# Kernel tuning notes

Measured on AMD Instinct MI355X. Metric: run time of the kernel, lower is better.

Reference implementation:

```python
import jax, jax.numpy as jnp
import numpy as np

VEC, HID, B, S = 1280, 128, 4, 256
EPS = 1e-5


def _ln(x):
    m = x.mean(-1, keepdims=True)
    v = ((x - m) ** 2).mean(-1, keepdims=True)
    return (x - m) / jnp.sqrt(v + EPS)


def _add_attn(q_in, kv_in, Wq, Wk, wv):
    # Additive (Bahdanau) attention: scores[b,i,j] = wv . tanh(q[b,i] + k[b,j])
    q = q_in @ Wq            # [B, Sq, H]
    k = kv_in @ Wk           # [B, Sk, H]
    feat = jnp.tanh(q[:, :, None, :] + k[:, None, :, :])   # [B, Sq, Sk, H]
    scores = jnp.einsum('bijh,h->bij', feat, wv)
    attn = jax.nn.softmax(scores, axis=-1)
    return jnp.einsum('bij,bjd->bid', attn, kv_in)          # values = kv_in


def _res_fc(x, W1, b1, W2, b2):
    return jnp.maximum(x @ W1 + b1, 0.0) @ W2 + b2 + x


def setup_inputs() -> dict:
    key = jax.random.key(0)
    ks = iter(jax.random.split(key, 64))
    d = {
        'X': jax.random.normal(next(ks), (B, S, VEC), dtype=jnp.float32),
        'lys_pos': 100,
    }
    sc = 0.02
    for i in (1, 2, 3, 4):
        d[f'Wq{i}'] = jax.random.normal(next(ks), (VEC, HID), dtype=jnp.float32) * sc
        d[f'Wk{i}'] = jax.random.normal(next(ks), (VEC, HID), dtype=jnp.float32) * sc
        d[f'wv{i}'] = jax.random.normal(next(ks), (HID,), dtype=jnp.float32) * sc
    for i in (1, 2, 3):
        d[f'rW1_{i}'] = jax.random.normal(next(ks), (VEC, HID), dtype=jnp.float32) * sc
        d[f'rb1_{i}'] = jnp.zeros((HID,), dtype=jnp.float32)
        d[f'rW2_{i}'] = jax.random.normal(next(ks), (HID, VEC), dtype=jnp.float32) * sc
        d[f'rb2_{i}'] = jnp.zeros((VEC,), dtype=jnp.float32)
    d['hW1'] = jax.random.normal(next(ks), (VEC, 32), dtype=jnp.float32) * sc
    d['hb1'] = jnp.zeros((32,), dtype=jnp.float32)
    d['hW2'] = jax.random.normal(next(ks), (32, 12), dtype=jnp.float32) * sc
    d['hb2'] = jnp.zeros((12,), dtype=jnp.float32)
    d['hW3'] = jax.random.normal(next(ks), (12, 2), dtype=jnp.float32) * sc
    d['hb3'] = jnp.zeros((2,), dtype=jnp.float32)
    return d


def reference(X, lys_pos,
              Wq1, Wk1, wv1, Wq2, Wk2, wv2, Wq3, Wk3, wv3, Wq4, Wk4, wv4,
              rW1_1, rb1_1, rW2_1, rb2_1,
              rW1_2, rb1_2, rW2_2, rb2_2,
              rW1_3, rb1_3, rW2_3, rb2_3,
              hW1, hb1, hW2, hb2, hW3, hb3):
    X = X.astype(jnp.float32)
    X = _ln(_add_attn(X, X, Wq1, Wk1, wv1) + X)
    X = _res_fc(X, rW1_1, rb1_1, rW2_1, rb2_1)
    X = _ln(_add_attn(X, X, Wq2, Wk2, wv2) + X)
    X = _res_fc(X, rW1_2, rb1_2, rW2_2, rb2_2)
    X = _ln(_add_attn(X, X, Wq3, Wk3, wv3) + X)
    X = _res_fc(X, rW1_3, rb1_3, rW2_3, rb2_3)
    X_lys = X[:, lys_pos, :][:, None, :]                    # [B, 1, VEC]
    X_lys = _ln(_add_attn(X_lys, X, Wq4, Wk4, wv4) + X_lys)
    h = jnp.maximum(X_lys @ hW1 + hb1, 0.0)                 # dropout = identity (eval)
    h = jnp.maximum(h @ hW2 + hb2, 0.0)
    logits = (h @ hW3 + hb3)[:, 0, :]                       # squeeze(1) -> [B, 2]
    return logits
```

## Files before the change

kernel.cpp:

```cpp
#include <hip/hip_runtime.h>


#define DEV __device__ __forceinline__

static constexpr int VEC = 1280;
static constexpr int HID = 128;
static constexpr int BB  = 4;
static constexpr int SS  = 256;
static constexpr int MROWS = BB * SS;
static constexpr int NPART = 8;

DEV float ftanh(float x) {
  float e = __expf(2.0f * x);
  return 1.0f - __fdividef(2.0f, e + 1.0f);
}

DEV float waveSum(float v) {
#pragma unroll
  for (int off = 32; off > 0; off >>= 1) v += __shfl_xor(v, off, 64);
  return v;
}
DEV float waveMax(float v) {
#pragma unroll
  for (int off = 32; off > 0; off >>= 1) v = fmaxf(v, __shfl_xor(v, off, 64));
  return v;
}
DEV float blockSum(float v, float* red) {
  v = waveSum(v);
  int tid = threadIdx.x;
  if ((tid & 63) == 0) red[tid >> 6] = v;
  __syncthreads();
  float r = (red[0] + red[1]) + (red[2] + red[3]);
  __syncthreads();
  return r;
}
DEV float blockMax(float v, float* red) {
  v = waveMax(v);
  int tid = threadIdx.x;
  if ((tid & 63) == 0) red[tid >> 6] = v;
  __syncthreads();
  float r = fmaxf(fmaxf(red[0], red[1]), fmaxf(red[2], red[3]));
  __syncthreads();
  return r;
}

template <int MODE, bool AFUSE, bool OBIAS, bool ORES>
__global__ __launch_bounds__(256) void gemm_k(
    const float* __restrict__ A, long sAb, long aPart,
    const float* __restrict__ B0, const float* __restrict__ B1, int nSplitB,
    long sBb, int ldB,
    float* __restrict__ C, long sCb,
    const float* __restrict__ aBias, const float* __restrict__ oBias,
    const float* __restrict__ res,
    int N, int K, int kChunk) {
  const int n0 = blockIdx.x * 64;
  const int m0 = blockIdx.y * 64;
  const int z  = blockIdx.z;

  const float* Ab = A + (MODE == 2 ? (long)z * sAb : 0L);
  float*       Cb = C + (MODE >= 1 ? (long)z * sCb : 0L);
  const float* resz = ORES ? (res + (MODE == 2 ? (long)z * sCb : 0L)) : nullptr;
  const float* Bsel;
  int nb;
  if (n0 < nSplitB) { Bsel = B0; nb = n0; } else { Bsel = B1; nb = n0 - nSplitB; }
  if (MODE == 2) Bsel += (long)z * sBb;

  const int kBeg = (MODE == 1) ? z * kChunk : 0;
  const int kEnd = (MODE == 1) ? kBeg + kChunk : K;

  __shared__ float As[16][68];
  __shared__ float Bs[16][68];

  const int tid = threadIdx.x;
  const int tx = tid & 15, ty = tid >> 4;
  const int ar = tid >> 2, ac = (tid & 3) << 2;
  const int br = tid >> 4, bc = (tid & 15) << 2;

  auto loadA = [&](int kt) -> float4 {
    const size_t aoff = (size_t)(m0 + ar) * K + kt + ac;
    if (AFUSE) {
      float4 s = *(const float4*)(Ab + aoff);
#pragma unroll
      for (int p = 1; p < NPART; ++p) {
        const float4 t = *(const float4*)(Ab + (long)p * aPart + aoff);
        s.x += t.x; s.y += t.y; s.z += t.z; s.w += t.w;
      }
      const float4 bz = *(const float4*)(aBias + kt + ac);
      s.x = fmaxf(s.x + bz.x, 0.0f);
      s.y = fmaxf(s.y + bz.y, 0.0f);
      s.z = fmaxf(s.z + bz.z, 0.0f);
      s.w = fmaxf(s.w + bz.w, 0.0f);
      return s;
    }
    return *(const float4*)(Ab + aoff);
  };
  auto loadB = [&](int kt) -> float4 {
    return *(const float4*)(Bsel + (size_t)(kt + br) * ldB + nb + bc);
  };

  float acc[4][4] = {};
  float4 a4 = loadA(kBeg);
  float4 b4 = loadB(kBeg);

  for (int kt = kBeg; kt < kEnd; kt += 16) {
    __syncthreads();
    As[ac + 0][ar] = a4.x;
    As[ac + 1][ar] = a4.y;
    As[ac + 2][ar] = a4.z;
    As[ac + 3][ar] = a4.w;
    *(float4*)&Bs[br][bc] = b4;
    __syncthreads();
    if (kt + 16 < kEnd) {
      a4 = loadA(kt + 16);
      b4 = loadB(kt + 16);
    }
#pragma unroll
    for (int kk = 0; kk < 16; ++kk) {
      const float4 av = *(const float4*)&As[kk][ty << 2];
      const float4 bv = *(const float4*)&Bs[kk][tx << 2];
      const float a[4] = {av.x, av.y, av.z, av.w};
      const float b[4] = {bv.x, bv.y, bv.z, bv.w};
#pragma unroll
      for (int i = 0; i < 4; ++i)
#pragma unroll
        for (int j = 0; j < 4; ++j) acc[i][j] = fmaf(a[i], b[j], acc[i][j]);
    }
  }

#pragma unroll
  for (int i = 0; i < 4; ++i) {
    const int m = m0 + (ty << 2) + i;
#pragma unroll
    for (int j = 0; j < 4; ++j) {
      const int n = n0 + (tx << 2) + j;
      float v = acc[i][j];
      if (OBIAS) v += oBias[n];
      if (ORES) v += resz[(size_t)m * N + n];
      Cb[(size_t)m * N + n] = v;
    }
  }
}

__global__ __launch_bounds__(256) void qksum_k(const float* __restrict__ QKp,
                                               long ps,
                                               float* __restrict__ Qd,
                                               float* __restrict__ KT) {
  const int r = blockIdx.x, tid = threadIdx.x;
  const int b = r >> 8, j = r & 255;
  const size_t off = (size_t)r * 256 + tid;
  float v = 0.0f;
#pragma unroll
  for (int p = 0; p < NPART; ++p) v += QKp[(long)p * ps + off];
  if (tid < 128) {
    Qd[(size_t)r * 128 + tid] = v;
  } else {
    KT[(size_t)b * 32768 + (size_t)(tid - 128) * 256 + j] = v;
  }
}

__global__ __launch_bounds__(256) void scores2_k(const float* __restrict__ Qd,
                                                 const float* __restrict__ KT,
                                                 const float* __restrict__ wv,
                                                 float* __restrict__ attn) {
  const int b = blockIdx.y, i0 = blockIdx.x * 2, tid = threadIdx.x;
  __shared__ float qs[2][128], wvs[128], red[4];
  {
    const int rr = tid >> 7, h = tid & 127;
    qs[rr][h] = Qd[(size_t)(b * 256 + i0 + rr) * 128 + h];
  }
  if (tid < 128) wvs[tid] = wv[tid];
  __syncthreads();

  const float* KTb = KT + (size_t)b * 32768 + tid;
  float s0 = 0.0f, s1 = 0.0f;
#pragma unroll 4
  for (int h = 0; h < 128; h += 4) {
    const float k0 = KTb[(h + 0) * 256];
    const float k1 = KTb[(h + 1) * 256];
    const float k2 = KTb[(h + 2) * 256];
    const float k3 = KTb[(h + 3) * 256];
    const float w0 = wvs[h], w1 = wvs[h + 1], w2 = wvs[h + 2], w3 = wvs[h + 3];
    s0 += w0 * ftanh(qs[0][h] + k0) + w1 * ftanh(qs[0][h + 1] + k1) +
          w2 * ftanh(qs[0][h + 2] + k2) + w3 * ftanh(qs[0][h + 3] + k3);
    s1 += w0 * ftanh(qs[1][h] + k0) + w1 * ftanh(qs[1][h + 1] + k1) +
          w2 * ftanh(qs[1][h + 2] + k2) + w3 * ftanh(qs[1][h + 3] + k3);
  }
  {
    const float mx = blockMax(s0, red);
    const float e = __expf(s0 - mx);
    const float tot = blockSum(e, red);
    attn[(size_t)(b * 256 + i0) * 256 + tid] = e / tot;
  }
  {
    const float mx = blockMax(s1, red);
    const float e = __expf(s1 - mx);
    const float tot = blockSum(e, red);
    attn[(size_t)(b * 256 + i0 + 1) * 256 + tid] = e / tot;
  }
}

__global__ __launch_bounds__(256) void ln1_k(const float* __restrict__ A,
                                             float* __restrict__ Y) {
  __shared__ float red[4];
  const int r = blockIdx.x, tid = threadIdx.x;
  const float* a = A + (size_t)r * VEC;
  float v[5];
  float sum = 0.0f;
#pragma unroll
  for (int k = 0; k < 5; ++k) {
    v[k] = a[tid + k * 256];
    sum += v[k];
  }
  sum = blockSum(sum, red);
  const float m = sum * (1.0f / VEC);
  float sq = 0.0f;
#pragma unroll
  for (int k = 0; k < 5; ++k) {
    const float dl = v[k] - m;
    sq += dl * dl;
  }
  sq = blockSum(sq, red);
  const float rstd = rsqrtf(sq * (1.0f / VEC) + 1e-5f);
  float* y = Y + (size_t)r * VEC;
#pragma unroll
  for (int k = 0; k < 5; ++k) y[tid + k * 256] = (v[k] - m) * rstd;
}

__global__ __launch_bounds__(256) void scores4_k(const float* __restrict__ Qd,
                                                 const float* __restrict__ KT,
                                                 const float* __restrict__ wv4,
                                                 const int* __restrict__ lys,
                                                 float* __restrict__ aw4) {
  const int b = blockIdx.x, tid = threadIdx.x;
  __shared__ float qs[128], wvs[128], red[4];
  const int lp = lys[0];
  if (tid < 128) {
    qs[tid] = Qd[(size_t)(b * 256 + lp) * 128 + tid];
    wvs[tid] = wv4[tid];
  }
  __syncthreads();
  const float* KTb = KT + (size_t)b * 32768 + tid;
  float s = 0.0f;
#pragma unroll 4
  for (int h = 0; h < 128; h += 4) {
    s += wvs[h + 0] * ftanh(qs[h + 0] + KTb[(h + 0) * 256]);
    s += wvs[h + 1] * ftanh(qs[h + 1] + KTb[(h + 1) * 256]);
    s += wvs[h + 2] * ftanh(qs[h + 2] + KTb[(h + 2) * 256]);
    s += wvs[h + 3] * ftanh(qs[h + 3] + KTb[(h + 3) * 256]);
  }
  const float mx = blockMax(s, red);
  const float e = __expf(s - mx);
  const float tot = blockSum(e, red);
  aw4[b * 256 + tid] = e / tot;
}

__global__ __launch_bounds__(256) void pv4_k(const float* __restrict__ aw4,
                                             const float* __restrict__ X3,
                                             const int* __restrict__ lys,
                                             float* __restrict__ A4) {
  const int b = blockIdx.x, c = blockIdx.y * 256 + threadIdx.x;
  __shared__ float aws[256];
  aws[threadIdx.x] = aw4[b * 256 + threadIdx.x];
  __syncthreads();
  const float* Xb = X3 + (size_t)b * SS * VEC;
  float acc = 0.0f;
#pragma unroll 8
  for (int j = 0; j < 256; ++j) acc = fmaf(aws[j], Xb[(size_t)j * VEC + c], acc);
  acc += Xb[(size_t)lys[0] * VEC + c];
  A4[b * VEC + c] = acc;
}

__global__ __launch_bounds__(256) void lnhead_k(
    const float* __restrict__ A4,
    const float* __restrict__ hW1, const float* __restrict__ hb1,
    const float* __restrict__ hW2, const float* __restrict__ hb2,
    const float* __restrict__ hW3, const float* __restrict__ hb3,
    float* __restrict__ out) {
  const int b = blockIdx.x, tid = threadIdx.x;
  __shared__ float xrow[1280], partial[256], red[4];
  __shared__ float h1s[32], h2s[12];
  float v[5];
  float sum = 0.0f;
#pragma unroll
  for (int k = 0; k < 5; ++k) {
    v[k] = A4[b * VEC + tid + k * 256];
    sum += v[k];
  }
  sum = blockSum(sum, red);
  const float m = sum * (1.0f / VEC);
  float sq = 0.0f;
#pragma unroll
  for (int k = 0; k < 5; ++k) {
    const float dl = v[k] - m;
    sq += dl * dl;
  }
  sq = blockSum(sq, red);
  const float rstd = rsqrtf(sq * (1.0f / VEC) + 1e-5f);
#pragma unroll
  for (int k = 0; k < 5; ++k) xrow[tid + k * 256] = (v[k] - m) * rstd;
  __syncthreads();
  {
    const int n = tid & 31, sl = tid >> 5;
    float p = 0.0f;
    for (int k = sl * 160; k < sl * 160 + 160; ++k)
      p = fmaf(xrow[k], hW1[(size_t)k * 32 + n], p);
    partial[tid] = p;
  }
  __syncthreads();
  if (tid < 32) {
    float t = 0.0f;
#pragma unroll
    for (int s2 = 0; s2 < 8; ++s2) t += partial[s2 * 32 + tid];
    h1s[tid] = fmaxf(t + hb1[tid], 0.0f);
  }
  __syncthreads();
  if (tid < 12) {
    float t = 0.0f;
#pragma unroll
    for (int k = 0; k < 32; ++k) t = fmaf(h1s[k], hW2[k * 12 + tid], t);
    h2s[tid] = fmaxf(t + hb2[tid], 0.0f);
  }
  __syncthreads();
  if (tid < 2) {
    float t = 0.0f;
#pragma unroll
    for (int k = 0; k < 12; ++k) t = fmaf(h2s[k], hW3[k * 2 + tid], t);
    out[b * 2 + tid] = t + hb3[tid];
  }
}

extern "C" void kernel_launch(void* const* d_in, const int* in_sizes, int n_in,
                              void* d_out, int out_size, void* d_ws, size_t ws_size,
                              hipStream_t stream) {
  const float* X = (const float*)d_in[0];
  const int* lys = (const int*)d_in[1];
  const float* Wq[4] = {(const float*)d_in[2], (const float*)d_in[5],
                        (const float*)d_in[8], (const float*)d_in[11]};
  const float* Wk[4] = {(const float*)d_in[3], (const float*)d_in[6],
                        (const float*)d_in[9], (const float*)d_in[12]};
  const float* wv[4] = {(const float*)d_in[4], (const float*)d_in[7],
                        (const float*)d_in[10], (const float*)d_in[13]};
  const float* rW1[3] = {(const float*)d_in[14], (const float*)d_in[18],
                         (const float*)d_in[22]};
  const float* rb1[3] = {(const float*)d_in[15], (const float*)d_in[19],
                         (const float*)d_in[23]};
  const float* rW2[3] = {(const float*)d_in[16], (const float*)d_in[20],
                         (const float*)d_in[24]};
  const float* rb2[3] = {(const float*)d_in[17], (const float*)d_in[21],
                         (const float*)d_in[25]};
  const float* hW1 = (const float*)d_in[26];
  const float* hb1 = (const float*)d_in[27];
  const float* hW2 = (const float*)d_in[28];
  const float* hb2 = (const float*)d_in[29];
  const float* hW3 = (const float*)d_in[30];
  const float* hb3 = (const float*)d_in[31];
  float* out = (float*)d_out;

  float* ws = (float*)d_ws;
  const long QK_PS = 262144;
  const long H_PS  = 131072;
  float* QKp  = ws;
  float* Qd   = QKp + (long)NPART * QK_PS;
  float* KT   = Qd + 131072;
  float* attn = KT + 131072;
  float* Yraw = attn + 262144;
  float* Yb   = Yraw + 1310720;
  float* Hp   = Yb + 1310720;
  float* buf0 = Hp + (long)NPART * H_PS;
  float* buf1 = buf0 + 1310720;
  float* aw4  = buf1 + 1310720;
  float* A4   = aw4 + 1024;

  const int NSPLIT_NONE = 1 << 30;
  const float* P[3] = {X, buf0, buf1};
  float* Q[3] = {buf0, buf1, buf0};

  for (int l = 0; l < 3; ++l) {
    const float* Xin = P[l];
    gemm_k<1, false, false, false><<<dim3(4, 16, NPART), 256, 0, stream>>>(
        Xin, 0, 0, Wq[l], Wk[l], HID, 0, HID, QKp, QK_PS, nullptr, nullptr,
        nullptr, 256, VEC, 160);
    qksum_k<<<dim3(MROWS), 256, 0, stream>>>(QKp, QK_PS, Qd, KT);
    scores2_k<<<dim3(128, BB), 256, 0, stream>>>(Qd, KT, wv[l], attn);
    gemm_k<2, false, false, true><<<dim3(20, 4, BB), 256, 0, stream>>>(
        attn, (long)SS * SS, 0, Xin, Xin, NSPLIT_NONE, (long)SS * VEC, VEC,
        Yraw, (long)SS * VEC, nullptr, nullptr, Xin, VEC, SS, 0);
    ln1_k<<<dim3(MROWS), 256, 0, stream>>>(Yraw, Yb);
    gemm_k<1, false, false, false><<<dim3(2, 16, NPART), 256, 0, stream>>>(
        Yb, 0, 0, rW1[l], rW1[l], NSPLIT_NONE, 0, HID, Hp, H_PS, nullptr,
        nullptr, nullptr, HID, VEC, 160);
    gemm_k<0, true, true, true><<<dim3(20, 16, 1), 256, 0, stream>>>(
        Hp, 0, H_PS, rW2[l], rW2[l], NSPLIT_NONE, 0, VEC, Q[l], 0, rb1[l],
        rb2[l], Yb, VEC, HID, 0);
  }

  const float* X3 = Q[2];
  gemm_k<1, false, false, false><<<dim3(4, 16, NPART), 256, 0, stream>>>(
      X3, 0, 0, Wq[3], Wk[3], HID, 0, HID, QKp, QK_PS, nullptr, nullptr,
      nullptr, 256, VEC, 160);
  qksum_k<<<dim3(MROWS), 256, 0, stream>>>(QKp, QK_PS, Qd, KT);
  scores4_k<<<dim3(BB), 256, 0, stream>>>(Qd, KT, wv[3], lys, aw4);
  pv4_k<<<dim3(BB, 5), 256, 0, stream>>>(aw4, X3, lys, A4);
  lnhead_k<<<dim3(BB), 256, 0, stream>>>(A4, hW1, hb1, hW2, hb2, hW3, hb3, out);
}
```

Measured before the change: 438.8 us.

## Fuse all stages into one persistent kernel with software grid barriers

Replaces about 30 separate kernel launches with a single persistent kernel of 512 blocks. Stages are separated by an atomic-counter grid barrier, and each block runs the matching tile tasks for the current stage. The tail stages (scores4, pv4, lnhead) are merged into one per-batch task. This removes launch gaps and inter-kernel drain at the cost of idle blocks in stages with fewer tiles, and it relies on all 512 blocks being co-resident to avoid deadlock.

```diff
diff --git a/kernel.cpp b/kernel.cpp
--- a/kernel.cpp
+++ b/kernel.cpp
@@ -7,8 +7,22 @@
 static constexpr int HID = 128;
 static constexpr int BB  = 4;
 static constexpr int SS  = 256;
-static constexpr int MROWS = BB * SS;
 static constexpr int NPART = 8;
+static constexpr long QK_PS = 262144;
+static constexpr long H_PS  = 131072;
+static constexpr int NBLK  = 512;
+static constexpr int NSPLIT_NONE = 1 << 30;
+
+struct Params {
+  const float* X; const int* lys;
+  const float* Wq[4]; const float* Wk[4]; const float* wv[4];
+  const float* rW1[3]; const float* rb1[3]; const float* rW2[3]; const float* rb2[3];
+  const float* hW1; const float* hb1; const float* hW2; const float* hb2;
+  const float* hW3; const float* hb3;
+  float* QKp; float* Qd; float* KT; float* attn; float* Yraw; float* Yb; float* Hp;
+  float* buf0; float* buf1; float* out;
+  unsigned* bar;
+};
 
 DEV float ftanh(float x) {
   float e = __expf(2.0f * x);
@@ -44,18 +58,39 @@
   return r;
 }
 
+DEV void gsync(unsigned* bar) {
+  __syncthreads();
+  if (threadIdx.x == 0) {
+    unsigned g = __hip_atomic_load(bar + 1, __ATOMIC_RELAXED,
+                                   __HIP_MEMORY_SCOPE_AGENT);
+    unsigned a = __hip_atomic_fetch_add(bar, 1u, __ATOMIC_ACQ_REL,
+                                        __HIP_MEMORY_SCOPE_AGENT);
+    if (a == (unsigned)(NBLK - 1)) {
+      __hip_atomic_store(bar, 0u, __ATOMIC_RELAXED, __HIP_MEMORY_SCOPE_AGENT);
+      __hip_atomic_store(bar + 1, g + 1u, __ATOMIC_RELEASE,
+                         __HIP_MEMORY_SCOPE_AGENT);
+    } else {
+      while (__hip_atomic_load(bar + 1, __ATOMIC_RELAXED,
+                               __HIP_MEMORY_SCOPE_AGENT) == g)
+        __builtin_amdgcn_s_sleep(4);
+      __builtin_amdgcn_fence(__ATOMIC_ACQUIRE, "agent");
+    }
+  }
+  __syncthreads();
+}
+
 template <int MODE, bool AFUSE, bool OBIAS, bool ORES>
-__global__ __launch_bounds__(256) void gemm_k(
-    const float* __restrict__ A, long sAb, long aPart,
-    const float* __restrict__ B0, const float* __restrict__ B1, int nSplitB,
-    long sBb, int ldB,
-    float* __restrict__ C, long sCb,
-    const float* __restrict__ aBias, const float* __restrict__ oBias,
-    const float* __restrict__ res,
-    int N, int K, int kChunk) {
-  const int n0 = blockIdx.x * 64;
-  const int m0 = blockIdx.y * 64;
-  const int z  = blockIdx.z;
+DEV void gemm_task(int n0, int m0, int z,
+                   const float* __restrict__ A, long sAb, long aPart,
+                   const float* __restrict__ B0, const float* __restrict__ B1,
+                   int nSplitB, long sBb, int ldB,
+                   float* __restrict__ C, long sCb,
+                   const float* __restrict__ aBias,
+                   const float* __restrict__ oBias,
+                   const float* __restrict__ res,
+                   int N, int K, int kChunk) {
+  __shared__ float As[16][68];
+  __shared__ float Bs[16][68];
 
   const float* Ab = A + (MODE == 2 ? (long)z * sAb : 0L);
   float*       Cb = C + (MODE >= 1 ? (long)z * sCb : 0L);
@@ -67,9 +102,6 @@
 
   const int kBeg = (MODE == 1) ? z * kChunk : 0;
   const int kEnd = (MODE == 1) ? kBeg + kChunk : K;
-
-  __shared__ float As[16][68];
-  __shared__ float Bs[16][68];
 
   const int tid = threadIdx.x;
   const int tx = tid & 15, ty = tid >> 4;
@@ -141,16 +173,14 @@
   }
 }
 
-__global__ __launch_bounds__(256) void qksum_k(const float* __restrict__ QKp,
-                                               long ps,
-                                               float* __restrict__ Qd,
-                                               float* __restrict__ KT) {
-  const int r = blockIdx.x, tid = threadIdx.x;
+DEV void qksum_task(int r, const float* __restrict__ QKp,
+                    float* __restrict__ Qd, float* __restrict__ KT) {
+  const int tid = threadIdx.x;
   const int b = r >> 8, j = r & 255;
   const size_t off = (size_t)r * 256 + tid;
   float v = 0.0f;
 #pragma unroll
-  for (int p = 0; p < NPART; ++p) v += QKp[(long)p * ps + off];
+  for (int p = 0; p < NPART; ++p) v += QKp[(long)p * QK_PS + off];
   if (tid < 128) {
     Qd[(size_t)r * 128 + tid] = v;
   } else {
@@ -158,11 +188,11 @@
   }
 }
 
-__global__ __launch_bounds__(256) void scores2_k(const float* __restrict__ Qd,
-                                                 const float* __restrict__ KT,
-                                                 const float* __restrict__ wv,
-                                                 float* __restrict__ attn) {
-  const int b = blockIdx.y, i0 = blockIdx.x * 2, tid = threadIdx.x;
+DEV void scores_task(int t, const float* __restrict__ Qd,
+                     const float* __restrict__ KT,
+                     const float* __restrict__ wv,
+                     float* __restrict__ attn) {
+  const int b = t >> 7, i0 = (t & 127) << 1, tid = threadIdx.x;
   __shared__ float qs[2][128], wvs[128], red[4];
   {
     const int rr = tid >> 7, h = tid & 127;
@@ -199,10 +229,9 @@
   }
 }
 
-__global__ __launch_bounds__(256) void ln1_k(const float* __restrict__ A,
-                                             float* __restrict__ Y) {
+DEV void ln_task(int r, const float* __restrict__ A, float* __restrict__ Y) {
   __shared__ float red[4];
-  const int r = blockIdx.x, tid = threadIdx.x;
+  const int tid = threadIdx.x;
   const float* a = A + (size_t)r * VEC;
   float v[5];
   float sum = 0.0f;
@@ -226,20 +255,20 @@
   for (int k = 0; k < 5; ++k) y[tid + k * 256] = (v[k] - m) * rstd;
 }
 
-__global__ __launch_bounds__(256) void scores4_k(const float* __restrict__ Qd,
-                                                 const float* __restrict__ KT,
-                                                 const float* __restrict__ wv4,
-                                                 const int* __restrict__ lys,
-                                                 float* __restrict__ aw4) {
-  const int b = blockIdx.x, tid = threadIdx.x;
-  __shared__ float qs[128], wvs[128], red[4];
-  const int lp = lys[0];
+DEV void tail_task(int b, const Params& p) {
+  __shared__ float qs[128], wvs[128], red[4], aws[256];
+  __shared__ float xrow[1280], partial[256];
+  __shared__ float h1s[32], h2s[12];
+  const int tid = threadIdx.x;
+  const int lp = p.lys[0];
+  const float* X3 = p.buf0;
+
   if (tid < 128) {
-    qs[tid] = Qd[(size_t)(b * 256 + lp) * 128 + tid];
-    wvs[tid] = wv4[tid];
-  }
-  __syncthreads();
-  const float* KTb = KT + (size_t)b * 32768 + tid;
+    qs[tid] = p.Qd[(size_t)(b * 256 + lp) * 128 + tid];
+    wvs[tid] = p.wv[3][tid];
+  }
+  __syncthreads();
+  const float* KTb = p.KT + (size_t)b * 32768 + tid;
   float s = 0.0f;
 #pragma unroll 4
   for (int h = 0; h < 128; h += 4) {
@@ -251,41 +280,22 @@
   const float mx = blockMax(s, red);
   const float e = __expf(s - mx);
   const float tot = blockSum(e, red);
-  aw4[b * 256 + tid] = e / tot;
-}
-
-__global__ __launch_bounds__(256) void pv4_k(const float* __restrict__ aw4,
-                                             const float* __restrict__ X3,
-                                             const int* __restrict__ lys,
-                                             float* __restrict__ A4) {
-  const int b = blockIdx.x, c = blockIdx.y * 256 + threadIdx.x;
-  __shared__ float aws[256];
-  aws[threadIdx.x] = aw4[b * 256 + threadIdx.x];
-  __syncthreads();
+  aws[tid] = e / tot;
+  __syncthreads();
+
   const float* Xb = X3 + (size_t)b * SS * VEC;
-  float acc = 0.0f;
-#pragma unroll 8
-  for (int j = 0; j < 256; ++j) acc = fmaf(aws[j], Xb[(size_t)j * VEC + c], acc);
-  acc += Xb[(size_t)lys[0] * VEC + c];
-  A4[b * VEC + c] = acc;
-}
-
-__global__ __launch_bounds__(256) void lnhead_k(
-    const float* __restrict__ A4,
-    const float* __restrict__ hW1, const float* __restrict__ hb1,
-    const float* __restrict__ hW2, const float* __restrict__ hb2,
-    const float* __restrict__ hW3, const float* __restrict__ hb3,
-    float* __restrict__ out) {
-  const int b = blockIdx.x, tid = threadIdx.x;
-  __shared__ float xrow[1280], partial[256], red[4];
-  __shared__ float h1s[32], h2s[12];
-  float v[5];
-  float sum = 0.0f;
-#pragma unroll
-  for (int k = 0; k < 5; ++k) {
-    v[k] = A4[b * VEC + tid + k * 256];
-    sum += v[k];
-  }
+  float v[5] = {};
+#pragma unroll 2
+  for (int j = 0; j < 256; ++j) {
+    const float aw = aws[j];
+    const float* xr = Xb + (size_t)j * VEC + tid;
+#pragma unroll
+    for (int k = 0; k < 5; ++k) v[k] = fmaf(aw, xr[k * 256], v[k]);
+  }
+#pragma unroll
+  for (int k = 0; k < 5; ++k) v[k] += Xb[(size_t)lp * VEC + tid + k * 256];
+
+  float sum = (v[0] + v[1]) + (v[2] + v[3]) + v[4];
   sum = blockSum(sum, red);
   const float m = sum * (1.0f / VEC);
   float sq = 0.0f;
@@ -299,107 +309,125 @@
 #pragma unroll
   for (int k = 0; k < 5; ++k) xrow[tid + k * 256] = (v[k] - m) * rstd;
   __syncthreads();
+
   {
     const int n = tid & 31, sl = tid >> 5;
-    float p = 0.0f;
+    float pacc = 0.0f;
     for (int k = sl * 160; k < sl * 160 + 160; ++k)
-      p = fmaf(xrow[k], hW1[(size_t)k * 32 + n], p);
-    partial[tid] = p;
+      pacc = fmaf(xrow[k], p.hW1[(size_t)k * 32 + n], pacc);
+    partial[tid] = pacc;
   }
   __syncthreads();
   if (tid < 32) {
-    float t = 0.0f;
-#pragma unroll
-    for (int s2 = 0; s2 < 8; ++s2) t += partial[s2 * 32 + tid];
-    h1s[tid] = fmaxf(t + hb1[tid], 0.0f);
+    float t2 = 0.0f;
+#pragma unroll
+    for (int s2 = 0; s2 < 8; ++s2) t2 += partial[s2 * 32 + tid];
+    h1s[tid] = fmaxf(t2 + p.hb1[tid], 0.0f);
   }
   __syncthreads();
   if (tid < 12) {
-    float t = 0.0f;
-#pragma unroll
-    for (int k = 0; k < 32; ++k) t = fmaf(h1s[k], hW2[k * 12 + tid], t);
-    h2s[tid] = fmaxf(t + hb2[tid], 0.0f);
+    float t2 = 0.0f;
+#pragma unroll
+    for (int k = 0; k < 32; ++k) t2 = fmaf(h1s[k], p.hW2[k * 12 + tid], t2);
+    h2s[tid] = fmaxf(t2 + p.hb2[tid], 0.0f);
   }
   __syncthreads();
   if (tid < 2) {
-    float t = 0.0f;
-#pragma unroll
-    for (int k = 0; k < 12; ++k) t = fmaf(h2s[k], hW3[k * 2 + tid], t);
-    out[b * 2 + tid] = t + hb3[tid];
-  }
+    float t2 = 0.0f;
+#pragma unroll
+    for (int k = 0; k < 12; ++k) t2 = fmaf(h2s[k], p.hW3[k * 2 + tid], t2);
+    p.out[b * 2 + tid] = t2 + p.hb3[tid];
+  }
+}
+
+__global__ __launch_bounds__(256, 2) void mega_k(Params p) {
+  const int bid = blockIdx.x;
+  const float* Pin[4]  = {p.X, p.buf0, p.buf1, p.buf0};
+  float*       Pout[3] = {p.buf0, p.buf1, p.buf0};
+
+  for (int l = 0; l < 4; ++l) {
+    const float* Xin = Pin[l];
+    {
+      const int x = bid & 3, y = (bid >> 2) & 15, z = bid >> 6;
+      gemm_task<1, false, false, false>(x * 64, y * 64, z, Xin, 0L, 0L,
+          p.Wq[l], p.Wk[l], HID, 0L, HID, p.QKp, QK_PS,
+          nullptr, nullptr, nullptr, 2 * HID, VEC, 160);
+    }
+    gsync(p.bar);
+    qksum_task(bid, p.QKp, p.Qd, p.KT);
+    qksum_task(bid + NBLK, p.QKp, p.Qd, p.KT);
+    gsync(p.bar);
+    if (l == 3) break;
+    scores_task(bid, p.Qd, p.KT, p.wv[l], p.attn);
+    gsync(p.bar);
+    if (bid < 320) {
+      const int x = bid % 20, y = (bid / 20) & 3, zb = bid / 80;
+      gemm_task<2, false, false, true>(x * 64, y * 64, zb, p.attn,
+          (long)SS * SS, 0L, Xin, Xin, NSPLIT_NONE, (long)SS * VEC, VEC,
+          p.Yraw, (long)SS * VEC, nullptr, nullptr, Xin, VEC, SS, 0);
+    }
+    gsync(p.bar);
+    ln_task(bid, p.Yraw, p.Yb);
+    ln_task(bid + NBLK, p.Yraw, p.Yb);
+    gsync(p.bar);
+    if (bid < 256) {
+      const int x = bid & 1, y = (bid >> 1) & 15, z = bid >> 5;
+      gemm_task<1, false, false, false>(x * 64, y * 64, z, p.Yb, 0L, 0L,
+          p.rW1[l], p.rW1[l], NSPLIT_NONE, 0L, HID, p.Hp, H_PS,
+          nullptr, nullptr, nullptr, HID, VEC, 160);
+    }
+    gsync(p.bar);
+    if (bid < 320) {
+      const int x = bid % 20, y = bid / 20;
+      gemm_task<0, true, true, true>(x * 64, y * 64, 0, p.Hp, 0L, H_PS,
+          p.rW2[l], p.rW2[l], NSPLIT_NONE, 0L, VEC, Pout[l], 0L,
+          p.rb1[l], p.rb2[l], p.Yb, VEC, HID, 0);
+    }
+    gsync(p.bar);
+  }
+  if (bid < BB) tail_task(bid, p);
+}
+
+__global__ void initbar_k(unsigned* __restrict__ bar) {
+  __hip_atomic_store(bar + 0, 0u, __ATOMIC_RELAXED, __HIP_MEMORY_SCOPE_SYSTEM);
+  __hip_atomic_store(bar + 1, 0u, __ATOMIC_RELAXED, __HIP_MEMORY_SCOPE_SYSTEM);
 }
 
 extern "C" void kernel_launch(void* const* d_in, const int* in_sizes, int n_in,
                               void* d_out, int out_size, void* d_ws, size_t ws_size,
                               hipStream_t stream) {
-  const float* X = (const float*)d_in[0];
-  const int* lys = (const int*)d_in[1];
-  const float* Wq[4] = {(const float*)d_in[2], (const float*)d_in[5],
-                        (const float*)d_in[8], (const float*)d_in[11]};
-  const float* Wk[4] = {(const float*)d_in[3], (const float*)d_in[6],
-                        (const float*)d_in[9], (const float*)d_in[12]};
-  const float* wv[4] = {(const float*)d_in[4], (const float*)d_in[7],
-                        (const float*)d_in[10], (const float*)d_in[13]};
-  const float* rW1[3] = {(const float*)d_in[14], (const float*)d_in[18],
-                         (const float*)d_in[22]};
-  const float* rb1[3] = {(const float*)d_in[15], (const float*)d_in[19],
-                         (const float*)d_in[23]};
-  const float* rW2[3] = {(const float*)d_in[16], (const float*)d_in[20],
-                         (const float*)d_in[24]};
-  const float* rb2[3] = {(const float*)d_in[17], (const float*)d_in[21],
-                         (const float*)d_in[25]};
-  const float* hW1 = (const float*)d_in[26];
-  const float* hb1 = (const float*)d_in[27];
-  const float* hW2 = (const float*)d_in[28];
-  const float* hb2 = (const float*)d_in[29];
-  const float* hW3 = (const float*)d_in[30];
-  const float* hb3 = (const float*)d_in[31];
-  float* out = (float*)d_out;
+  Params p;
+  p.X   = (const float*)d_in[0];
+  p.lys = (const int*)d_in[1];
+  p.Wq[0] = (const float*)d_in[2];  p.Wk[0] = (const float*)d_in[3];  p.wv[0] = (const float*)d_in[4];
+  p.Wq[1] = (const float*)d_in[5];  p.Wk[1] = (const float*)d_in[6];  p.wv[1] = (const float*)d_in[7];
+  p.Wq[2] = (const float*)d_in[8];  p.Wk[2] = (const float*)d_in[9];  p.wv[2] = (const float*)d_in[10];
+  p.Wq[3] = (const float*)d_in[11]; p.Wk[3] = (const float*)d_in[12]; p.wv[3] = (const float*)d_in[13];
+  p.rW1[0] = (const float*)d_in[14]; p.rb1[0] = (const float*)d_in[15];
+  p.rW2[0] = (const float*)d_in[16]; p.rb2[0] = (const float*)d_in[17];
+  p.rW1[1] = (const float*)d_in[18]; p.rb1[1] = (const float*)d_in[19];
+  p.rW2[1] = (const float*)d_in[20]; p.rb2[1] = (const float*)d_in[21];
+  p.rW1[2] = (const float*)d_in[22]; p.rb1[2] = (const float*)d_in[23];
+  p.rW2[2] = (const float*)d_in[24]; p.rb2[2] = (const float*)d_in[25];
+  p.hW1 = (const float*)d_in[26]; p.hb1 = (const float*)d_in[27];
+  p.hW2 = (const float*)d_in[28]; p.hb2 = (const float*)d_in[29];
+  p.hW3 = (const float*)d_in[30]; p.hb3 = (const float*)d_in[31];
+  p.out = (float*)d_out;
 
   float* ws = (float*)d_ws;
-  const long QK_PS = 262144;
-  const long H_PS  = 131072;
-  float* QKp  = ws;
-  float* Qd   = QKp + (long)NPART * QK_PS;
-  float* KT   = Qd + 131072;
-  float* attn = KT + 131072;
-  float* Yraw = attn + 262144;
-  float* Yb   = Yraw + 1310720;
-  float* Hp   = Yb + 1310720;
-  float* buf0 = Hp + (long)NPART * H_PS;
-  float* buf1 = buf0 + 1310720;
-  float* aw4  = buf1 + 1310720;
-  float* A4   = aw4 + 1024;
-
-  const int NSPLIT_NONE = 1 << 30;
-  const float* P[3] = {X, buf0, buf1};
-  float* Q[3] = {buf0, buf1, buf0};
-
-  for (int l = 0; l < 3; ++l) {
-    const float* Xin = P[l];
-    gemm_k<1, false, false, false><<<dim3(4, 16, NPART), 256, 0, stream>>>(
-        Xin, 0, 0, Wq[l], Wk[l], HID, 0, HID, QKp, QK_PS, nullptr, nullptr,
-        nullptr, 256, VEC, 160);
-    qksum_k<<<dim3(MROWS), 256, 0, stream>>>(QKp, QK_PS, Qd, KT);
-    scores2_k<<<dim3(128, BB), 256, 0, stream>>>(Qd, KT, wv[l], attn);
-    gemm_k<2, false, false, true><<<dim3(20, 4, BB), 256, 0, stream>>>(
-        attn, (long)SS * SS, 0, Xin, Xin, NSPLIT_NONE, (long)SS * VEC, VEC,
-        Yraw, (long)SS * VEC, nullptr, nullptr, Xin, VEC, SS, 0);
-    ln1_k<<<dim3(MROWS), 256, 0, stream>>>(Yraw, Yb);
-    gemm_k<1, false, false, false><<<dim3(2, 16, NPART), 256, 0, stream>>>(
-        Yb, 0, 0, rW1[l], rW1[l], NSPLIT_NONE, 0, HID, Hp, H_PS, nullptr,
-        nullptr, nullptr, HID, VEC, 160);
-    gemm_k<0, true, true, true><<<dim3(20, 16, 1), 256, 0, stream>>>(
-        Hp, 0, H_PS, rW2[l], rW2[l], NSPLIT_NONE, 0, VEC, Q[l], 0, rb1[l],
-        rb2[l], Yb, VEC, HID, 0);
-  }
-
-  const float* X3 = Q[2];
-  gemm_k<1, false, false, false><<<dim3(4, 16, NPART), 256, 0, stream>>>(
-      X3, 0, 0, Wq[3], Wk[3], HID, 0, HID, QKp, QK_PS, nullptr, nullptr,
-      nullptr, 256, VEC, 160);
-  qksum_k<<<dim3(MROWS), 256, 0, stream>>>(QKp, QK_PS, Qd, KT);
-  scores4_k<<<dim3(BB), 256, 0, stream>>>(Qd, KT, wv[3], lys, aw4);
-  pv4_k<<<dim3(BB, 5), 256, 0, stream>>>(aw4, X3, lys, A4);
-  lnhead_k<<<dim3(BB), 256, 0, stream>>>(A4, hW1, hb1, hW2, hb2, hW3, hb3, out);
-}
+  p.QKp  = ws;
+  p.Qd   = p.QKp + (long)NPART * QK_PS;
+  p.KT   = p.Qd + 131072;
+  p.attn = p.KT + 131072;
+  p.Yraw = p.attn + 262144;
+  p.Yb   = p.Yraw + 1310720;
+  p.Hp   = p.Yb + 1310720;
+  p.buf0 = p.Hp + (long)NPART * H_PS;
+  p.buf1 = p.buf0 + 1310720;
+  float* aw4 = p.buf1 + 1310720;
+  float* A4  = aw4 + 1024;
+  p.bar = (unsigned*)(A4 + 4 * VEC);
+
+  initbar_k<<<dim3(1), dim3(1), 0, stream>>>(p.bar);
+  mega_k<<<dim3(NBLK), dim3(256), 0, stream>>>(p);
+}
```

Result: slower. 1.493 ms (+240.3%).
